# Kernel optimization log

Measured on AMD Instinct MI355X. Metric: run time of the kernel, lower is better.

## Reference

```python
import jax, jax.numpy as jnp
import numpy as np

EMBED_DIM = 1024
NUM_HEADS = 16
BATCH = 4
SEQ = 2048
HEAD_DIM = EMBED_DIM // NUM_HEADS


def get_alibi_slope(num_heads):
    x = (2 ** 8) ** (1 / num_heads)
    slope = jnp.array([1 / x ** (i + 1) for i in range(num_heads)], dtype=jnp.float32)
    return slope[:, None, None]  # [H,1,1]


def setup_inputs() -> dict:
    key = jax.random.key(0)
    k1, k2, k3 = jax.random.split(key, 3)
    x = jax.random.normal(k1, (BATCH, SEQ, EMBED_DIM), dtype=jnp.float32)
    # causal mask, broadcastable to [B,H,S,S]
    mask = jnp.tril(jnp.ones((SEQ, SEQ), dtype=bool))[None, None, :, :]
    W_qkv = jax.random.normal(k2, (EMBED_DIM, 3 * EMBED_DIM), dtype=jnp.float32) * (EMBED_DIM ** -0.5)
    b_qkv = jnp.zeros((3 * EMBED_DIM,), dtype=jnp.float32)
    W_out = jax.random.normal(k3, (EMBED_DIM, EMBED_DIM), dtype=jnp.float32) * (EMBED_DIM ** -0.5)
    b_out = jnp.zeros((EMBED_DIM,), dtype=jnp.float32)
    return {"x": x, "mask": mask, "W_qkv": W_qkv, "b_qkv": b_qkv, "W_out": W_out, "b_out": b_out}


def reference(x, mask, W_qkv, b_qkv, W_out, b_out):
    B, S, E = x.shape
    H, D = NUM_HEADS, HEAD_DIM
    qkv = x @ W_qkv + b_qkv                     # [B,S,3E]
    qkv = qkv.reshape(B, S, 3, H, D)
    q, k, v = qkv[:, :, 0], qkv[:, :, 1], qkv[:, :, 2]  # each [B,S,H,D]
    scores = jnp.einsum('bqhd,bkhd->bhqk', q, k) / jnp.sqrt(jnp.asarray(D, x.dtype))
    # ALiBi bias: slope[h] * (k_pos - q_pos)
    rel = (jnp.arange(S)[None, :] - jnp.arange(S)[:, None]).astype(x.dtype)  # [S,S]
    scores = scores + get_alibi_slope(H).astype(x.dtype) * rel               # broadcast [H,S,S]
    scores = jnp.where(mask, scores, jnp.asarray(-1e9, x.dtype))
    attn = jax.nn.softmax(scores, axis=-1)       # [B,H,S,S]
    out = jnp.einsum('bhqk,bkhd->bqhd', attn, v).reshape(B, S, E)
    return out @ W_out + b_out
```

## Files before the change

### kernel.cpp

```cpp
#include <hip/hip_runtime.h>
#include <hip/hip_bf16.h>
#include <cstdint>
#include <cstddef>

#define BATCH  4
#define SEQ    2048
#define EMBED  1024
#define NHEADS 16
#define HDIM   64

typedef __attribute__((ext_vector_type(8))) short  short8;
typedef __attribute__((ext_vector_type(4))) float  floatx4;

#define MASK_NEG (-1.0e30f)
#define LOG2E    1.44269504f

__device__ __forceinline__ float bf2f(ushort u) {
  union { uint32_t i; float f; } v; v.i = ((uint32_t)u) << 16; return v.f;
}
__device__ __forceinline__ ushort f2bf(float f) {
  union { float f; uint32_t i; } v; v.f = f;
  uint32_t u = v.i;
  return (ushort)((u + 0x7fffu + ((u >> 16) & 1u)) >> 16);
}
__device__ __forceinline__ uint32_t f2bf_pk(float a, float b) {
  union { __hip_bfloat162 h; uint32_t u; } v;
  v.h = __float22bfloat162_rn(make_float2(a, b));
  return v.u;
}
__device__ __forceinline__ void gll16(const ushort* g, ushort* l) {
  __builtin_amdgcn_global_load_lds(
      (const __attribute__((address_space(1))) void*)g,
      (__attribute__((address_space(3))) void*)l, 16, 0, 0);
}

__global__ __launch_bounds__(256) void detect_dtype(
    const uint32_t* __restrict__ x, int* __restrict__ flag) {
  __shared__ int sh[256];
  int tid = threadIdx.x;
  int c = 0;
#pragma unroll
  for (int i = 0; i < 16; i++) {
    uint32_t w = x[tid * 16 + i];
    uint32_t lo = w & 0xFFFFu;
    int e = (int)((lo >> 7) & 0xFF);
    if (lo == 0u || (e >= 100 && e <= 140)) c++;
  }
  sh[tid] = c;
  __syncthreads();
  if (tid == 0) {
    int s = 0;
    for (int i = 0; i < 256; i++) s += sh[i];
    *flag = (s >= 3500) ? 1 : 0;
  }
}

__global__ __launch_bounds__(256) void cvt_bf16_v4(
    const void* __restrict__ in, ushort* __restrict__ out,
    const int* __restrict__ flag, int n4) {
  bool isbf = (*flag != 0);
  int stride = gridDim.x * 256;
  for (int i = blockIdx.x * 256 + threadIdx.x; i < n4; i += stride) {
    if (isbf) {
      ((uint2*)out)[i] = ((const uint2*)in)[i];
    } else {
      float4 f = ((const float4*)in)[i];
      uint2 o;
      o.x = f2bf_pk(f.x, f.y);
      o.y = f2bf_pk(f.z, f.w);
      ((uint2*)out)[i] = o;
    }
  }
}

__global__ __launch_bounds__(256) void cvt_biases(
    const void* __restrict__ bq, const void* __restrict__ bo,
    ushort* __restrict__ bqb, ushort* __restrict__ bob,
    const int* __restrict__ flag) {
  bool isbf = (*flag != 0);
  int i = blockIdx.x * 256 + threadIdx.x;
  if (i < 3 * EMBED) {
    bqb[i] = isbf ? ((const ushort*)bq)[i] : f2bf(((const float*)bq)[i]);
  } else {
    int j = i - 3 * EMBED;
    bob[j] = isbf ? ((const ushort*)bo)[j] : f2bf(((const float*)bo)[j]);
  }
}

__global__ __launch_bounds__(256) void transpose_cvt(
    const void* __restrict__ in, ushort* __restrict__ out,
    const int* __restrict__ flag, int R, int C) {
  bool isbf = (*flag != 0);
  __shared__ ushort tile[32][33];
  int bx = blockIdx.x * 32;
  int by = blockIdx.y * 32;
  int tx = threadIdx.x & 31, ty = threadIdx.x >> 5;
#pragma unroll
  for (int i = 0; i < 32; i += 8) {
    size_t idx = (size_t)(by + ty + i) * C + bx + tx;
    tile[ty + i][tx] = isbf ? ((const ushort*)in)[idx] : f2bf(((const float*)in)[idx]);
  }
  __syncthreads();
#pragma unroll
  for (int i = 0; i < 32; i += 8)
    out[(size_t)(bx + ty + i) * R + by + tx] = tile[tx][ty + i];
}

__global__ __launch_bounds__(256) void transpose_v(
    const ushort* __restrict__ in, ushort* __restrict__ out) {
  __shared__ ushort tile[32][33];
  int bh = blockIdx.z;
  int s0 = blockIdx.x * 32;
  int d0 = blockIdx.y * 32;
  int tx = threadIdx.x & 31, ty = threadIdx.x >> 5;
  const ushort* ip = in + (size_t)bh * SEQ * HDIM;
  ushort* op = out + (size_t)bh * SEQ * HDIM;
#pragma unroll
  for (int i = 0; i < 32; i += 8)
    tile[ty + i][tx] = ip[(size_t)(s0 + ty + i) * HDIM + d0 + tx];
  __syncthreads();
#pragma unroll
  for (int i = 0; i < 32; i += 8)
    op[(size_t)(d0 + ty + i) * SEQ + s0 + tx] = tile[tx][ty + i];
}

template <int EPI>
__global__ __launch_bounds__(256) void gemm128(
    const ushort* __restrict__ A, const ushort* __restrict__ BT,
    const ushort* __restrict__ bias,
    ushort* __restrict__ out0, ushort* __restrict__ out1, ushort* __restrict__ out2,
    const int* __restrict__ flag,
    int M, int N, int K) {
  __shared__ __align__(16) ushort Al[128 * 64];
  __shared__ __align__(16) ushort Bl[128 * 64];

  const int tid  = threadIdx.x;
  const int lane = tid & 63, wave = tid >> 6;
  const int quad = lane >> 4, l15 = lane & 15;
  const int wm = wave >> 1, wn = wave & 1;
  const int rowA0 = blockIdx.y * 128;
  const int colB0 = blockIdx.x * 128;

  floatx4 acc[4][4] = {};

  int srow[4], sc8[4];
#pragma unroll
  for (int j = 0; j < 4; j++) {
    int s = tid + j * 256;
    srow[j] = s >> 3;
    sc8[j] = ((s & 7) ^ (srow[j] & 7)) * 8;
  }

  for (int kk = 0; kk < K; kk += 64) {
    __syncthreads();
#pragma unroll
    for (int j = 0; j < 4; j++)
      gll16(&A[(size_t)(rowA0 + srow[j]) * K + kk + sc8[j]], &Al[(tid + j * 256) * 8]);
#pragma unroll
    for (int j = 0; j < 4; j++)
      gll16(&BT[(size_t)(colB0 + srow[j]) * K + kk + sc8[j]], &Bl[(tid + j * 256) * 8]);
    __syncthreads();

#pragma unroll
    for (int h = 0; h < 2; h++) {
      short8 af[4], bf[4];
#pragma unroll
      for (int mt = 0; mt < 4; mt++) {
        int row = wm * 64 + mt * 16 + l15;
        int pos = (quad + 4 * h) ^ (l15 & 7);
        af[mt] = *(const short8*)&Al[row * 64 + pos * 8];
      }
#pragma unroll
      for (int nt = 0; nt < 4; nt++) {
        int row = wn * 64 + nt * 16 + l15;
        int pos = (quad + 4 * h) ^ (l15 & 7);
        bf[nt] = *(const short8*)&Bl[row * 64 + pos * 8];
      }
#pragma unroll
      for (int mt = 0; mt < 4; mt++)
#pragma unroll
        for (int nt = 0; nt < 4; nt++)
          acc[mt][nt] = __builtin_amdgcn_mfma_f32_16x16x32_bf16(af[mt], bf[nt], acc[mt][nt], 0, 0, 0);
    }
  }

  const bool isbf = (EPI == 1) ? (*flag != 0) : true;

#pragma unroll
  for (int mt = 0; mt < 4; mt++)
#pragma unroll
    for (int nt = 0; nt < 4; nt++)
#pragma unroll
      for (int r = 0; r < 4; r++) {
        int row = rowA0 + wm * 64 + mt * 16 + quad * 4 + r;
        int col = colB0 + wn * 64 + nt * 16 + l15;
        float v = acc[mt][nt][r] + bf2f(bias[col]);
        if (EPI == 0) {
          int three = col >> 10, rem = col & 1023, h = rem >> 6, d = rem & 63;
          int b = row >> 11, s = row & 2047;
          ushort* dst = (three == 0) ? out0 : (three == 1) ? out1 : out2;
          dst[((size_t)(b * NHEADS + h) * SEQ + s) * HDIM + d] = f2bf(v);
        } else {
          if (isbf) out0[(size_t)row * N + col] = f2bf(v);
          else      ((float*)out0)[(size_t)row * N + col] = v;
        }
      }
}

__global__ __launch_bounds__(256, 2) void attn_kernel(
    const ushort* __restrict__ Q, const ushort* __restrict__ K,
    const ushort* __restrict__ VT, ushort* __restrict__ Oout) {
  __shared__ __align__(16) ushort Kl[2][64 * 72];
  __shared__ __align__(16) ushort Vt[2][64 * 72];
  __shared__ __align__(16) ushort Pl[4][32 * 72];

  const int tid  = threadIdx.x;
  const int lane = tid & 63, wave = tid >> 6;
  const int quad = lane >> 4, l15 = lane & 15;
  const int pair = blockIdx.x;
  const int h = blockIdx.y, b = blockIdx.z;
  const int bh = b * NHEADS + h;
  const ushort* Qp  = Q  + (size_t)bh * SEQ * HDIM;
  const ushort* Kp  = K  + (size_t)bh * SEQ * HDIM;
  const ushort* VTp = VT + (size_t)bh * SEQ * HDIM;

  const float slope2 = exp2f(-0.5f * (float)(h + 1)) * LOG2E;
  const float c2 = 0.125f * LOG2E;
  float rt[4];
#pragma unroll
  for (int r = 0; r < 4; r++) rt[r] = slope2 * (float)r;

  const int sr0 = tid >> 3,         so0 = (tid & 7) * 8;
  const int sr1 = (tid + 256) >> 3, so1 = (tid & 7) * 8;

  for (int qsel = 0; qsel < 2; qsel++) {
    const int qt = qsel ? (15 - pair) : pair;
    const int wq0 = qt * 128 + wave * 32;
    const int wqmax = wq0 + 31;

    short8 qf[2][2];
#pragma unroll
    for (int mf = 0; mf < 2; mf++) {
      const ushort* qr = &Qp[(size_t)(wq0 + mf * 16 + l15) * HDIM];
      qf[mf][0] = *(const short8*)&qr[quad * 8];
      qf[mf][1] = *(const short8*)&qr[32 + quad * 8];
    }

    float m2s[2] = {MASK_NEG, MASK_NEG}, lis[2] = {0.f, 0.f};
    float qrowf[2];
#pragma unroll
    for (int mf = 0; mf < 2; mf++) qrowf[mf] = (float)(wq0 + mf * 16 + l15);
    floatx4 o_acc[2][4] = {};

    uint4 pk0 = *(const uint4*)&Kp[(size_t)sr0 * HDIM + so0];
    uint4 pk1 = *(const uint4*)&Kp[(size_t)sr1 * HDIM + so1];
    uint4 pv0 = *(const uint4*)&VTp[(size_t)sr0 * SEQ + so0];
    uint4 pv1 = *(const uint4*)&VTp[(size_t)sr1 * SEQ + so1];
    __syncthreads();
    *(uint4*)&Kl[0][sr0 * 72 + so0] = pk0;
    *(uint4*)&Kl[0][sr1 * 72 + so1] = pk1;
    *(uint4*)&Vt[0][sr0 * 72 + so0] = pv0;
    *(uint4*)&Vt[0][sr1 * 72 + so1] = pv1;
    __syncthreads();

    const int ntiles = 2 * qt + 2;
    for (int kt = 0; kt < ntiles; kt++) {
      const int kb = kt * 64;
      const int cur = kt & 1;
      const bool more = (kt + 1 < ntiles);

      if (more) {
        const int kb2 = kb + 64;
        pk0 = *(const uint4*)&Kp[(size_t)(kb2 + sr0) * HDIM + so0];
        pk1 = *(const uint4*)&Kp[(size_t)(kb2 + sr1) * HDIM + so1];
        pv0 = *(const uint4*)&VTp[(size_t)sr0 * SEQ + kb2 + so0];
        pv1 = *(const uint4*)&VTp[(size_t)sr1 * SEQ + kb2 + so1];
      }

      if (kb <= wqmax) {
#pragma unroll
        for (int mf = 0; mf < 2; mf++) {
          floatx4 sm[4];
#pragma unroll
          for (int kct = 0; kct < 4; kct++) {
            short8 a0 = *(const short8*)&Kl[cur][(kct * 16 + l15) * 72 + quad * 8];
            short8 a1 = *(const short8*)&Kl[cur][(kct * 16 + l15) * 72 + 32 + quad * 8];
            floatx4 z = {};
            z = __builtin_amdgcn_mfma_f32_16x16x32_bf16(a0, qf[mf][0], z, 0, 0, 0);
            sm[kct] = __builtin_amdgcn_mfma_f32_16x16x32_bf16(a1, qf[mf][1], z, 0, 0, 0);
          }

          const bool needs_mask = (kb + 63 > wq0 + mf * 16);
          float mloc = MASK_NEG;
#pragma unroll
          for (int kct = 0; kct < 4; kct++) {
            float keyb = (float)(kb + kct * 16 + quad * 4);
            float base = slope2 * keyb;
#pragma unroll
            for (int r = 0; r < 4; r++) {
              float v = fmaf(sm[kct][r], c2, base + rt[r]);
              if (needs_mask && (keyb + (float)r > qrowf[mf])) v = MASK_NEG;
              sm[kct][r] = v;
              mloc = fmaxf(mloc, v);
            }
          }
          mloc = fmaxf(mloc, __shfl_xor(mloc, 16, 64));
          mloc = fmaxf(mloc, __shfl_xor(mloc, 32, 64));

          float mn = fmaxf(m2s[mf], mloc);
          float al = exp2f(m2s[mf] - mn);
          m2s[mf] = mn;

          float rs = 0.f;
#pragma unroll
          for (int kct = 0; kct < 4; kct++) {
            float p0 = exp2f(sm[kct][0] - mn), p1 = exp2f(sm[kct][1] - mn);
            float p2 = exp2f(sm[kct][2] - mn), p3 = exp2f(sm[kct][3] - mn);
            rs += (p0 + p1) + (p2 + p3);
            uint2 pw;
            pw.x = f2bf_pk(p0, p1);
            pw.y = f2bf_pk(p2, p3);
            *(uint2*)&Pl[wave][(mf * 16 + l15) * 72 + kct * 16 + quad * 4] = pw;
          }
          rs += __shfl_xor(rs, 16, 64);
          rs += __shfl_xor(rs, 32, 64);
          lis[mf] = lis[mf] * al + rs;

          float alr[4];
#pragma unroll
          for (int r = 0; r < 4; r++) alr[r] = __shfl(al, quad * 4 + r, 16);
#pragma unroll
          for (int ct = 0; ct < 4; ct++)
#pragma unroll
            for (int r = 0; r < 4; r++) o_acc[mf][ct][r] *= alr[r];
        }

#pragma unroll
        for (int ks = 0; ks < 2; ks++) {
          short8 vf[4];
#pragma unroll
          for (int ct = 0; ct < 4; ct++)
            vf[ct] = *(const short8*)&Vt[cur][(ct * 16 + l15) * 72 + ks * 32 + quad * 8];
#pragma unroll
          for (int mf = 0; mf < 2; mf++) {
            short8 pf = *(const short8*)&Pl[wave][(mf * 16 + l15) * 72 + ks * 32 + quad * 8];
#pragma unroll
            for (int ct = 0; ct < 4; ct++)
              o_acc[mf][ct] = __builtin_amdgcn_mfma_f32_16x16x32_bf16(pf, vf[ct], o_acc[mf][ct], 0, 0, 0);
          }
        }
      }

      if (more) {
        const int nxt = cur ^ 1;
        *(uint4*)&Kl[nxt][sr0 * 72 + so0] = pk0;
        *(uint4*)&Kl[nxt][sr1 * 72 + so1] = pk1;
        *(uint4*)&Vt[nxt][sr0 * 72 + so0] = pv0;
        *(uint4*)&Vt[nxt][sr1 * 72 + so1] = pv1;
      }
      __syncthreads();
    }

#pragma unroll
    for (int mf = 0; mf < 2; mf++) {
      float inv = 1.0f / fmaxf(lis[mf], 1e-20f);
      float invr[4];
#pragma unroll
      for (int r = 0; r < 4; r++) invr[r] = __shfl(inv, quad * 4 + r, 16);
#pragma unroll
      for (int ct = 0; ct < 4; ct++)
#pragma unroll
        for (int r = 0; r < 4; r++) {
          int q = wq0 + mf * 16 + quad * 4 + r;
          float v = o_acc[mf][ct][r] * invr[r];
          Oout[(size_t)(b * SEQ + q) * EMBED + h * HDIM + ct * 16 + l15] = f2bf(v);
        }
    }
  }
}

extern "C" void kernel_launch(void* const* d_in, const int* in_sizes, int n_in,
                              void* d_out, int out_size, void* d_ws, size_t ws_size,
                              hipStream_t stream) {
  const void* x     = d_in[0];
  const void* W_qkv = d_in[2];
  const void* b_qkv = d_in[3];
  const void* W_out = d_in[4];
  const void* b_out = d_in[5];

  char* ws = (char*)d_ws;
  int*    flag = (int*)(ws + 0);
  ushort* xb   = (ushort*)(ws + 1024);
  ushort* WTq  = (ushort*)(ws + 16778240);
  ushort* WTo  = (ushort*)(ws + 23069696);
  ushort* bqb  = (ushort*)(ws + 25166848);
  ushort* bob  = (ushort*)(ws + 25172992);
  ushort* Kw   = (ushort*)(ws + 25175040);
  ushort* Vw   = (ushort*)(ws + 41952256);
  ushort* VTw  = (ushort*)(ws + 58729472);
  ushort* Aw   = Vw;
  ushort* Qw   = (ws_size >= (size_t)75506688 + 16777216)
                   ? (ushort*)(ws + 75506688)
                   : (ushort*)d_out;

  detect_dtype<<<1, 256, 0, stream>>>((const uint32_t*)x, flag);

  cvt_bf16_v4<<<2048, 256, 0, stream>>>(x, xb, flag, BATCH * SEQ * EMBED / 4);
  cvt_biases<<<16, 256, 0, stream>>>(b_qkv, b_out, bqb, bob, flag);

  transpose_cvt<<<dim3(3072 / 32, 1024 / 32), 256, 0, stream>>>(W_qkv, WTq, flag, 1024, 3072);
  transpose_cvt<<<dim3(1024 / 32, 1024 / 32), 256, 0, stream>>>(W_out, WTo, flag, 1024, 1024);

  gemm128<0><<<dim3(3072 / 128, 8192 / 128), 256, 0, stream>>>(
      xb, WTq, bqb, Qw, Kw, Vw, flag, BATCH * SEQ, 3 * EMBED, EMBED);

  transpose_v<<<dim3(SEQ / 32, HDIM / 32, BATCH * NHEADS), 256, 0, stream>>>(Vw, VTw);

  attn_kernel<<<dim3(SEQ / 256, NHEADS, BATCH), 256, 0, stream>>>(Qw, Kw, VTw, Aw);

  gemm128<1><<<dim3(1024 / 128, 8192 / 128), 256, 0, stream>>>(
      Aw, WTo, bob, (ushort*)d_out, nullptr, nullptr, flag, BATCH * SEQ, EMBED, EMBED);
}
```

Before: 321.1 us.

## Shrink attention query tile, swizzle LDS, and remap blocks per XCD

Each attention block now handles a 64-row query tile (16 rows per wave) instead of 128, which doubles the grid to 1024 blocks, cuts registers per wave, and raises the launch-bounds occupancy target from 2 to 4. The padded LDS rows (stride 72) are replaced with XOR-swizzled 64-wide rows so LDS use shrinks while bank conflicts are still avoided. Block indices are remapped so that all query tiles of the same batch-head land on the same XCD, aiming for better L2 reuse of K/V. The trade-off is that K/V tiles are loaded from global memory twice as often per query row, and each wave issues less MFMA work per K/V tile load.

```diff
diff --git a/kernel.cpp b/kernel.cpp
--- a/kernel.cpp
+++ b/kernel.cpp
@@ -207,19 +207,24 @@
       }
 }
 
-__global__ __launch_bounds__(256, 2) void attn_kernel(
+__global__ __launch_bounds__(256, 4) void attn_kernel(
     const ushort* __restrict__ Q, const ushort* __restrict__ K,
     const ushort* __restrict__ VT, ushort* __restrict__ Oout) {
-  __shared__ __align__(16) ushort Kl[2][64 * 72];
-  __shared__ __align__(16) ushort Vt[2][64 * 72];
-  __shared__ __align__(16) ushort Pl[4][32 * 72];
+  __shared__ __align__(16) ushort Kl[2][64 * 64];
+  __shared__ __align__(16) ushort Vt[2][64 * 64];
+  __shared__ __align__(16) ushort Pl[4][16 * 64];
 
   const int tid  = threadIdx.x;
   const int lane = tid & 63, wave = tid >> 6;
   const int quad = lane >> 4, l15 = lane & 15;
-  const int pair = blockIdx.x;
-  const int h = blockIdx.y, b = blockIdx.z;
-  const int bh = b * NHEADS + h;
+
+  const int L   = blockIdx.x + 16 * blockIdx.y + 256 * blockIdx.z;
+  const int xcd = L & 7;
+  const int idx = L >> 3;
+  const int bh  = xcd * 8 + (idx >> 4);
+  const int p   = idx & 15;
+  const int h   = bh & 15, b = bh >> 4;
+
   const ushort* Qp  = Q  + (size_t)bh * SEQ * HDIM;
   const ushort* Kp  = K  + (size_t)bh * SEQ * HDIM;
   const ushort* VTp = VT + (size_t)bh * SEQ * HDIM;
@@ -230,40 +235,40 @@
 #pragma unroll
   for (int r = 0; r < 4; r++) rt[r] = slope2 * (float)r;
 
-  const int sr0 = tid >> 3,         so0 = (tid & 7) * 8;
-  const int sr1 = (tid + 256) >> 3, so1 = (tid & 7) * 8;
+  const int sr0 = tid >> 3, sr1 = sr0 + 32;
+  const int sc  = tid & 7;
+  const int so  = sc * 8;
+  const int sw0 = sr0 * 64 + (sc ^ (sr0 & 7)) * 8;
+  const int sw1 = sr1 * 64 + (sc ^ (sr0 & 7)) * 8;
+  const int sxr = l15 & 7;
 
   for (int qsel = 0; qsel < 2; qsel++) {
-    const int qt = qsel ? (15 - pair) : pair;
-    const int wq0 = qt * 128 + wave * 32;
-    const int wqmax = wq0 + 31;
-
-    short8 qf[2][2];
-#pragma unroll
-    for (int mf = 0; mf < 2; mf++) {
-      const ushort* qr = &Qp[(size_t)(wq0 + mf * 16 + l15) * HDIM];
-      qf[mf][0] = *(const short8*)&qr[quad * 8];
-      qf[mf][1] = *(const short8*)&qr[32 + quad * 8];
+    const int qt  = qsel ? (31 - p) : p;
+    const int wq0 = qt * 64 + wave * 16;
+
+    short8 qf0, qf1;
+    {
+      const ushort* qr = &Qp[(size_t)(wq0 + l15) * HDIM];
+      qf0 = *(const short8*)&qr[quad * 8];
+      qf1 = *(const short8*)&qr[32 + quad * 8];
     }
 
-    float m2s[2] = {MASK_NEG, MASK_NEG}, lis[2] = {0.f, 0.f};
-    float qrowf[2];
-#pragma unroll
-    for (int mf = 0; mf < 2; mf++) qrowf[mf] = (float)(wq0 + mf * 16 + l15);
-    floatx4 o_acc[2][4] = {};
-
-    uint4 pk0 = *(const uint4*)&Kp[(size_t)sr0 * HDIM + so0];
-    uint4 pk1 = *(const uint4*)&Kp[(size_t)sr1 * HDIM + so1];
-    uint4 pv0 = *(const uint4*)&VTp[(size_t)sr0 * SEQ + so0];
-    uint4 pv1 = *(const uint4*)&VTp[(size_t)sr1 * SEQ + so1];
+    float m2 = MASK_NEG, li = 0.f;
+    const float qrowf = (float)(wq0 + l15);
+    floatx4 o_acc[4] = {};
+
+    uint4 pk0 = *(const uint4*)&Kp[(size_t)sr0 * HDIM + so];
+    uint4 pk1 = *(const uint4*)&Kp[(size_t)sr1 * HDIM + so];
+    uint4 pv0 = *(const uint4*)&VTp[(size_t)sr0 * SEQ + so];
+    uint4 pv1 = *(const uint4*)&VTp[(size_t)sr1 * SEQ + so];
     __syncthreads();
-    *(uint4*)&Kl[0][sr0 * 72 + so0] = pk0;
-    *(uint4*)&Kl[0][sr1 * 72 + so1] = pk1;
-    *(uint4*)&Vt[0][sr0 * 72 + so0] = pv0;
-    *(uint4*)&Vt[0][sr1 * 72 + so1] = pv1;
+    *(uint4*)&Kl[0][sw0] = pk0;
+    *(uint4*)&Kl[0][sw1] = pk1;
+    *(uint4*)&Vt[0][sw0] = pv0;
+    *(uint4*)&Vt[0][sw1] = pv1;
     __syncthreads();
 
-    const int ntiles = 2 * qt + 2;
+    const int ntiles = qt + 1;
     for (int kt = 0; kt < ntiles; kt++) {
       const int kb = kt * 64;
       const int cur = kt & 1;
@@ -271,99 +276,91 @@
 
       if (more) {
         const int kb2 = kb + 64;
-        pk0 = *(const uint4*)&Kp[(size_t)(kb2 + sr0) * HDIM + so0];
-        pk1 = *(const uint4*)&Kp[(size_t)(kb2 + sr1) * HDIM + so1];
-        pv0 = *(const uint4*)&VTp[(size_t)sr0 * SEQ + kb2 + so0];
-        pv1 = *(const uint4*)&VTp[(size_t)sr1 * SEQ + kb2 + so1];
-      }
-
-      if (kb <= wqmax) {
-#pragma unroll
-        for (int mf = 0; mf < 2; mf++) {
-          floatx4 sm[4];
-#pragma unroll
-          for (int kct = 0; kct < 4; kct++) {
-            short8 a0 = *(const short8*)&Kl[cur][(kct * 16 + l15) * 72 + quad * 8];
-            short8 a1 = *(const short8*)&Kl[cur][(kct * 16 + l15) * 72 + 32 + quad * 8];
-            floatx4 z = {};
-            z = __builtin_amdgcn_mfma_f32_16x16x32_bf16(a0, qf[mf][0], z, 0, 0, 0);
-            sm[kct] = __builtin_amdgcn_mfma_f32_16x16x32_bf16(a1, qf[mf][1], z, 0, 0, 0);
-          }
-
-          const bool needs_mask = (kb + 63 > wq0 + mf * 16);
-          float mloc = MASK_NEG;
-#pragma unroll
-          for (int kct = 0; kct < 4; kct++) {
-            float keyb = (float)(kb + kct * 16 + quad * 4);
-            float base = slope2 * keyb;
-#pragma unroll
-            for (int r = 0; r < 4; r++) {
-              float v = fmaf(sm[kct][r], c2, base + rt[r]);
-              if (needs_mask && (keyb + (float)r > qrowf[mf])) v = MASK_NEG;
-              sm[kct][r] = v;
-              mloc = fmaxf(mloc, v);
-            }
-          }
-          mloc = fmaxf(mloc, __shfl_xor(mloc, 16, 64));
-          mloc = fmaxf(mloc, __shfl_xor(mloc, 32, 64));
-
-          float mn = fmaxf(m2s[mf], mloc);
-          float al = exp2f(m2s[mf] - mn);
-          m2s[mf] = mn;
-
-          float rs = 0.f;
-#pragma unroll
-          for (int kct = 0; kct < 4; kct++) {
-            float p0 = exp2f(sm[kct][0] - mn), p1 = exp2f(sm[kct][1] - mn);
-            float p2 = exp2f(sm[kct][2] - mn), p3 = exp2f(sm[kct][3] - mn);
-            rs += (p0 + p1) + (p2 + p3);
-            uint2 pw;
-            pw.x = f2bf_pk(p0, p1);
-            pw.y = f2bf_pk(p2, p3);
-            *(uint2*)&Pl[wave][(mf * 16 + l15) * 72 + kct * 16 + quad * 4] = pw;
-          }
-          rs += __shfl_xor(rs, 16, 64);
-          rs += __shfl_xor(rs, 32, 64);
-          lis[mf] = lis[mf] * al + rs;
-
-          float alr[4];
-#pragma unroll
-          for (int r = 0; r < 4; r++) alr[r] = __shfl(al, quad * 4 + r, 16);
-#pragma unroll
-          for (int ct = 0; ct < 4; ct++)
-#pragma unroll
-            for (int r = 0; r < 4; r++) o_acc[mf][ct][r] *= alr[r];
+        pk0 = *(const uint4*)&Kp[(size_t)(kb2 + sr0) * HDIM + so];
+        pk1 = *(const uint4*)&Kp[(size_t)(kb2 + sr1) * HDIM + so];
+        pv0 = *(const uint4*)&VTp[(size_t)sr0 * SEQ + kb2 + so];
+        pv1 = *(const uint4*)&VTp[(size_t)sr1 * SEQ + kb2 + so];
+      }
+
+      floatx4 sm[4];
+#pragma unroll
+      for (int kct = 0; kct < 4; kct++) {
+        const ushort* kr = &Kl[cur][(kct * 16 + l15) * 64];
+        short8 a0 = *(const short8*)&kr[(quad ^ sxr) * 8];
+        short8 a1 = *(const short8*)&kr[((quad + 4) ^ sxr) * 8];
+        floatx4 z = {};
+        z = __builtin_amdgcn_mfma_f32_16x16x32_bf16(a0, qf0, z, 0, 0, 0);
+        sm[kct] = __builtin_amdgcn_mfma_f32_16x16x32_bf16(a1, qf1, z, 0, 0, 0);
+      }
+
+      const bool needs_mask = (kb + 63 > wq0);
+      float mloc = MASK_NEG;
+#pragma unroll
+      for (int kct = 0; kct < 4; kct++) {
+        float keyb = (float)(kb + kct * 16 + quad * 4);
+        float base = slope2 * keyb;
+#pragma unroll
+        for (int r = 0; r < 4; r++) {
+          float v = fmaf(sm[kct][r], c2, base + rt[r]);
+          if (needs_mask && (keyb + (float)r > qrowf)) v = MASK_NEG;
+          sm[kct][r] = v;
+          mloc = fmaxf(mloc, v);
         }
-
-#pragma unroll
-        for (int ks = 0; ks < 2; ks++) {
-          short8 vf[4];
-#pragma unroll
-          for (int ct = 0; ct < 4; ct++)
-            vf[ct] = *(const short8*)&Vt[cur][(ct * 16 + l15) * 72 + ks * 32 + quad * 8];
-#pragma unroll
-          for (int mf = 0; mf < 2; mf++) {
-            short8 pf = *(const short8*)&Pl[wave][(mf * 16 + l15) * 72 + ks * 32 + quad * 8];
-#pragma unroll
-            for (int ct = 0; ct < 4; ct++)
-              o_acc[mf][ct] = __builtin_amdgcn_mfma_f32_16x16x32_bf16(pf, vf[ct], o_acc[mf][ct], 0, 0, 0);
-          }
-        }
+      }
+      mloc = fmaxf(mloc, __shfl_xor(mloc, 16, 64));
+      mloc = fmaxf(mloc, __shfl_xor(mloc, 32, 64));
+
+      float mn = fmaxf(m2, mloc);
+      float al = exp2f(m2 - mn);
+      m2 = mn;
+
+      float rs = 0.f;
+#pragma unroll
+      for (int kct = 0; kct < 4; kct++) {
+        float p0 = exp2f(sm[kct][0] - mn), p1 = exp2f(sm[kct][1] - mn);
+        float p2 = exp2f(sm[kct][2] - mn), p3 = exp2f(sm[kct][3] - mn);
+        rs += (p0 + p1) + (p2 + p3);
+        uint2 pw;
+        pw.x = f2bf_pk(p0, p1);
+        pw.y = f2bf_pk(p2, p3);
+        *(uint2*)&Pl[wave][l15 * 64 + ((kct * 2 + (quad >> 1)) ^ sxr) * 8 + (quad & 1) * 4] = pw;
+      }
+      rs += __shfl_xor(rs, 16, 64);
+      rs += __shfl_xor(rs, 32, 64);
+      li = li * al + rs;
+
+      float alr[4];
+#pragma unroll
+      for (int r = 0; r < 4; r++) alr[r] = __shfl(al, quad * 4 + r, 16);
+#pragma unroll
+      for (int ct = 0; ct < 4; ct++)
+#pragma unroll
+        for (int r = 0; r < 4; r++) o_acc[ct][r] *= alr[r];
+
+#pragma unroll
+      for (int ks = 0; ks < 2; ks++) {
+        short8 vf[4];
+#pragma unroll
+        for (int ct = 0; ct < 4; ct++)
+          vf[ct] = *(const short8*)&Vt[cur][(ct * 16 + l15) * 64 + ((ks * 4 + quad) ^ sxr) * 8];
+        short8 pf = *(const short8*)&Pl[wave][l15 * 64 + ((ks * 4 + quad) ^ sxr) * 8];
+#pragma unroll
+        for (int ct = 0; ct < 4; ct++)
+          o_acc[ct] = __builtin_amdgcn_mfma_f32_16x16x32_bf16(pf, vf[ct], o_acc[ct], 0, 0, 0);
       }
 
       if (more) {
         const int nxt = cur ^ 1;
-        *(uint4*)&Kl[nxt][sr0 * 72 + so0] = pk0;
-        *(uint4*)&Kl[nxt][sr1 * 72 + so1] = pk1;
-        *(uint4*)&Vt[nxt][sr0 * 72 + so0] = pv0;
-        *(uint4*)&Vt[nxt][sr1 * 72 + so1] = pv1;
+        *(uint4*)&Kl[nxt][sw0] = pk0;
+        *(uint4*)&Kl[nxt][sw1] = pk1;
+        *(uint4*)&Vt[nxt][sw0] = pv0;
+        *(uint4*)&Vt[nxt][sw1] = pv1;
       }
       __syncthreads();
     }
 
-#pragma unroll
-    for (int mf = 0; mf < 2; mf++) {
-      float inv = 1.0f / fmaxf(lis[mf], 1e-20f);
+    {
+      float inv = 1.0f / fmaxf(li, 1e-20f);
       float invr[4];
 #pragma unroll
       for (int r = 0; r < 4; r++) invr[r] = __shfl(inv, quad * 4 + r, 16);
@@ -371,8 +368,8 @@
       for (int ct = 0; ct < 4; ct++)
 #pragma unroll
         for (int r = 0; r < 4; r++) {
-          int q = wq0 + mf * 16 + quad * 4 + r;
-          float v = o_acc[mf][ct][r] * invr[r];
+          int q = wq0 + quad * 4 + r;
+          float v = o_acc[ct][r] * invr[r];
           Oout[(size_t)(b * SEQ + q) * EMBED + h * HDIM + ct * 16 + l15] = f2bf(v);
         }
     }
@@ -416,7 +413,7 @@
 
   transpose_v<<<dim3(SEQ / 32, HDIM / 32, BATCH * NHEADS), 256, 0, stream>>>(Vw, VTw);
 
-  attn_kernel<<<dim3(SEQ / 256, NHEADS, BATCH), 256, 0, stream>>>(Qw, Kw, VTw, Aw);
+  attn_kernel<<<dim3(16, 16, 4), 256, 0, stream>>>(Qw, Kw, VTw, Aw);
 
   gemm128<1><<<dim3(1024 / 128, 8192 / 128), 256, 0, stream>>>(
       Aw, WTo, bob, (ushort*)d_out, nullptr, nullptr, flag, BATCH * SEQ, EMBED, EMBED);
```

Result: no change. 314.9 us (-2.0%).
